# Performance work log

Hardware: AMD Instinct MI355X
Metric: run time of the kernel (lower is better)

The kernel has to match this reference:

```python
import jax, jax.numpy as jnp
import numpy as np

B, Q, K = 8, 1024, 1024
DQ, DK, DV, H = 64, 64, 64, 64
NEG = -1000000.0


def setup_inputs() -> dict:
    key = jax.random.key(0)
    ks = jax.random.split(key, 7)
    return {
        "queries": jax.random.normal(ks[0], (B, Q, DQ), dtype=jnp.float32),
        "keys": jax.random.normal(ks[1], (B, K, DK), dtype=jnp.float32),
        "values": jax.random.normal(ks[2], (B, K, DV), dtype=jnp.float32),
        "valid_lens": jax.random.randint(ks[3], (B,), 1, K + 1, dtype=jnp.int64).astype(jnp.int32),
        # learned params (LazyLinear, no bias)
        "W_q": jax.random.normal(ks[4], (DQ, H), dtype=jnp.float32) / np.sqrt(DQ),
        "W_k": jax.random.normal(ks[5], (DK, H), dtype=jnp.float32) / np.sqrt(DK),
        "w_v": jax.random.normal(ks[6], (H,), dtype=jnp.float32) / np.sqrt(H),
    }


def reference(queries, keys, values, valid_lens, W_q, W_k, w_v):
    q = jnp.einsum("bqd,dh->bqh", queries, W_q)            # [B,Q,H]
    k = jnp.einsum("bkd,dh->bkh", keys, W_k)               # [B,K,H]
    # broadcast-add + tanh materializes [B,Q,K,H] (faithful to original)
    features = jnp.tanh(q[:, :, None, :] + k[:, None, :, :])
    scores = jnp.einsum("bqkh,h->bqk", features, w_v)      # [B,Q,K]
    # masked softmax: valid_lens is 1-D -> broadcast over query rows
    mask = jnp.arange(scores.shape[-1])[None, None, :] < valid_lens[:, None, None]
    scores = jnp.where(mask, scores, NEG)
    attn = jax.nn.softmax(scores, axis=-1)                 # [B,Q,K]
    return jnp.einsum("bqk,bkv->bqv", attn, values)        # [B,Q,DV]
```

## Files before the change

kernel.cpp:

```cpp
#include <hip/hip_runtime.h>

#define BDIM 8
#define QDIM 1024
#define KDIM 1024
#define HDIM 64
#define KTPC 2
#define MAXCH 8

constexpr float kLog2e = 1.4426950408889634f;
constexpr float kC2 = 2.0f * kLog2e;

__global__ __launch_bounds__(256) void proj_both(
    const float* __restrict__ queries, const float* __restrict__ keys,
    const float* __restrict__ Wq, const float* __restrict__ Wk,
    float* __restrict__ eq, float* __restrict__ ek) {
  const int bid = blockIdx.x;
  const bool isK = bid >= 256;
  const float* X = isK ? keys : queries;
  const float* W = isK ? Wk : Wq;
  float* Y = isK ? ek : eq;
  const long long base = (long long)(bid & 255) * 32 * 64;

  __shared__ __align__(16) float xs[32][68];
  __shared__ __align__(16) float ws[64][64];
  const int t = threadIdx.x;
  {
    const int r = t >> 4, sl = t & 15;
#pragma unroll
    for (int i = 0; i < 2; ++i)
      *(float4*)&xs[r + i * 16][sl * 4] =
          *(const float4*)&X[base + (long long)(r + i * 16) * 64 + sl * 4];
#pragma unroll
    for (int i = 0; i < 4; ++i)
      *(float4*)&ws[r + i * 16][sl * 4] =
          *(const float4*)&W[(r + i * 16) * 64 + sl * 4];
  }
  __syncthreads();

  const int r = t >> 3;
  const int c0 = (t & 7) * 8;
  float acc[8];
#pragma unroll
  for (int j = 0; j < 8; ++j) acc[j] = 0.0f;

#pragma unroll 8
  for (int d = 0; d < 64; ++d) {
    const float xv = xs[r][d];
#pragma unroll
    for (int j4 = 0; j4 < 2; ++j4) {
      float4 w4 = *(float4*)&ws[d][c0 + j4 * 4];
      acc[j4 * 4 + 0] = fmaf(xv, w4.x, acc[j4 * 4 + 0]);
      acc[j4 * 4 + 1] = fmaf(xv, w4.y, acc[j4 * 4 + 1]);
      acc[j4 * 4 + 2] = fmaf(xv, w4.z, acc[j4 * 4 + 2]);
      acc[j4 * 4 + 3] = fmaf(xv, w4.w, acc[j4 * 4 + 3]);
    }
  }
#pragma unroll
  for (int j4 = 0; j4 < 2; ++j4) {
    float4 o = make_float4(
        fminf(__builtin_amdgcn_exp2f(acc[j4 * 4 + 0] * kC2), 32768.0f),
        fminf(__builtin_amdgcn_exp2f(acc[j4 * 4 + 1] * kC2), 32768.0f),
        fminf(__builtin_amdgcn_exp2f(acc[j4 * 4 + 2] * kC2), 32768.0f),
        fminf(__builtin_amdgcn_exp2f(acc[j4 * 4 + 3] * kC2), 32768.0f));
    *(float4*)&Y[base + (long long)r * 64 + c0 + j4 * 4] = o;
  }
}

__global__ __launch_bounds__(256, 4) void fused_kernel(
    const float* __restrict__ eqp, const float* __restrict__ ekp,
    const float* __restrict__ vglob, const float* __restrict__ wv,
    const int* __restrict__ vlens, float* __restrict__ part_o,
    float* __restrict__ part_l) {
  int pre[9];
  pre[0] = 0;
#pragma unroll
  for (int bb = 0; bb < 8; ++bb) {
    int nt = (vlens[bb] + 63) >> 6;
    nt = nt < 16 ? nt : 16;
    const int nch = (nt + KTPC - 1) / KTPC;
    pre[bb + 1] = pre[bb] + (nch << 6);
  }
  const int g = blockIdx.x;
  if (g >= pre[8]) return;
  int b = 0;
#pragma unroll
  for (int i = 0; i < 7; ++i) b += (g >= pre[i + 1]);
  const int local = g - pre[b];
  const int qt = local & 63;
  const int ch = local >> 6;
  const int q0 = qt * 16;
  const int vlen = vlens[b];
  int nt = (vlen + 63) >> 6;
  nt = nt < 16 ? nt : 16;
  const int kt0 = ch * KTPC;
  const int ktend = (kt0 + KTPC < nt) ? kt0 + KTPC : nt;

  __shared__ __align__(16) float qs[16][64];
  __shared__ __align__(16) float ks[64][64];
  __shared__ __align__(16) float vs[64][64];
  __shared__ __align__(16) float ps[16][64];
  const int t = threadIdx.x;
  const int tq = t >> 4;
  const int kg = t & 15;
  const int kbs = kg << 2;
  const int key0 = ((kbs + 0) ^ kg) & 15;
  const int key1 = ((kbs + 1) ^ kg) & 15;
  const int key2 = ((kbs + 2) ^ kg) & 15;
  const int key3 = ((kbs + 3) ^ kg) & 15;

  float sumw = 0.0f, sumabs = 0.0f;
#pragma unroll
  for (int h = 0; h < 64; ++h) {
    const float w = wv[h];
    sumw += w;
    sumabs += fabsf(w);
  }
  const float sbias = sumw - sumabs;

  {
    const int r = t >> 4, sl = t & 15;
    *(float4*)&qs[r][sl * 4] =
        *(const float4*)&eqp[(long long)(b * QDIM + q0 + r) * 64 + sl * 4];
  }

  float4 o4 = make_float4(0.0f, 0.0f, 0.0f, 0.0f);
  float l = 0.0f;

  for (int kt = kt0; kt < ktend; ++kt) {
    __syncthreads();
#pragma unroll
    for (int i = 0; i < 4; ++i) {
      const int f = i * 256 + t;
      const int k = f >> 4, sl = f & 15;
      const int key = (k ^ (k >> 2)) & 15;
      const long long grow = (long long)(b * KDIM + kt * 64 + k) * 64 + sl * 4;
      *(float4*)&ks[k][(sl ^ key) * 4] = *(const float4*)&ekp[grow];
      *(float4*)&vs[k][sl * 4] = *(const float4*)&vglob[grow];
    }
    __syncthreads();

    float acc0 = 0.0f, acc1 = 0.0f, acc2 = 0.0f, acc3 = 0.0f;
    float4 qA, kA0, kA1, kA2, kA3;
    float4 qB, kB0, kB1, kB2, kB3;

#define LOAD_STAGE(QF, K0, K1, K2, K3, H)                  \
  QF = *(const float4*)&qs[tq][(H) * 4];                   \
  K0 = *(const float4*)&ks[kbs + 0][((H) ^ key0) * 4];     \
  K1 = *(const float4*)&ks[kbs + 1][((H) ^ key1) * 4];     \
  K2 = *(const float4*)&ks[kbs + 2][((H) ^ key2) * 4];     \
  K3 = *(const float4*)&ks[kbs + 3][((H) ^ key3) * 4];

#define QUAD(ACC, QF, KF, W0, W1, W2, W3)                  \
  {                                                        \
    const float u0 = fmaf(QF.x, KF.x, 1.0f);               \
    const float u1 = fmaf(QF.y, KF.y, 1.0f);               \
    const float u2 = fmaf(QF.z, KF.z, 1.0f);               \
    const float u3 = fmaf(QF.w, KF.w, 1.0f);               \
    const float d01 = u0 * u1;                             \
    const float d23 = u2 * u3;                             \
    const float n01 = fmaf(W1, u0, W0 * u1);               \
    const float n23 = fmaf(W3, u2, W2 * u3);               \
    const float num = fmaf(n23, d01, n01 * d23);           \
    ACC = fmaf(num, __builtin_amdgcn_rcpf(d01 * d23), ACC);\
  }

#define COMP_STAGE(QF, K0, K1, K2, K3, H)                  \
  {                                                        \
    const float w0 = wv[(H) * 4 + 0];                      \
    const float w1 = wv[(H) * 4 + 1];                      \
    const float w2 = wv[(H) * 4 + 2];                      \
    const float w3 = wv[(H) * 4 + 3];                      \
    QUAD(acc0, QF, K0, w0, w1, w2, w3)                     \
    QUAD(acc1, QF, K1, w0, w1, w2, w3)                     \
    QUAD(acc2, QF, K2, w0, w1, w2, w3)                     \
    QUAD(acc3, QF, K3, w0, w1, w2, w3)                     \
  }

    LOAD_STAGE(qA, kA0, kA1, kA2, kA3, 0)
#pragma unroll
    for (int h = 0; h < 16; h += 2) {
      LOAD_STAGE(qB, kB0, kB1, kB2, kB3, h + 1)
      COMP_STAGE(qA, kA0, kA1, kA2, kA3, h)
      if (h + 2 < 16) LOAD_STAGE(qA, kA0, kA1, kA2, kA3, h + 2)
      COMP_STAGE(qB, kB0, kB1, kB2, kB3, h + 1)
    }
#undef LOAD_STAGE
#undef COMP_STAGE
#undef QUAD

    const int kgl = kt * 64 + kbs;
    float s0 = fmaf(-2.0f, acc0, sbias);
    float s1 = fmaf(-2.0f, acc1, sbias);
    float s2 = fmaf(-2.0f, acc2, sbias);
    float s3 = fmaf(-2.0f, acc3, sbias);
    s0 = (kgl + 0 < vlen) ? s0 : -3.0e38f;
    s1 = (kgl + 1 < vlen) ? s1 : -3.0e38f;
    s2 = (kgl + 2 < vlen) ? s2 : -3.0e38f;
    s3 = (kgl + 3 < vlen) ? s3 : -3.0e38f;
    const float p0 = __builtin_amdgcn_exp2f(s0 * kLog2e);
    const float p1 = __builtin_amdgcn_exp2f(s1 * kLog2e);
    const float p2 = __builtin_amdgcn_exp2f(s2 * kLog2e);
    const float p3 = __builtin_amdgcn_exp2f(s3 * kLog2e);
    l += (p0 + p1) + (p2 + p3);
    *(float4*)&ps[tq][(((kg + tq) & 15)) * 4] = make_float4(p0, p1, p2, p3);

#pragma unroll 4
    for (int k4 = 0; k4 < 16; ++k4) {
      const int kk = (k4 + tq) & 15;
      const float4 p4 = *(const float4*)&ps[tq][((kk + tq) & 15) * 4];
      const float pw[4] = {p4.x, p4.y, p4.z, p4.w};
#pragma unroll
      for (int e = 0; e < 4; ++e) {
        const float4 vv = *(const float4*)&vs[kk * 4 + e][kbs];
        o4.x = fmaf(pw[e], vv.x, o4.x);
        o4.y = fmaf(pw[e], vv.y, o4.y);
        o4.z = fmaf(pw[e], vv.z, o4.z);
        o4.w = fmaf(pw[e], vv.w, o4.w);
      }
    }
  }

#pragma unroll
  for (int s = 1; s < 16; s <<= 1) l += __shfl_xor(l, s, 64);
  *(float4*)&part_o[((long long)g * 16 + tq) * 64 + kbs] = o4;
  if (kg == 0) part_l[g * 16 + tq] = l;
}

__global__ __launch_bounds__(256) void combine_kernel(
    const float* __restrict__ part_o, const float* __restrict__ part_l,
    const int* __restrict__ vlens, float* __restrict__ out) {
  int pre[8], nchv[8];
  int run = 0;
#pragma unroll
  for (int bb = 0; bb < 8; ++bb) {
    int nt = (vlens[bb] + 63) >> 6;
    nt = nt < 16 ? nt : 16;
    nchv[bb] = (nt + KTPC - 1) / KTPC;
    pre[bb] = run;
    run += nchv[bb] << 6;
  }
  const int t = threadIdx.x;
  const int row = blockIdx.x * 4 + (t >> 6);
  const int lane = t & 63;
  const int b = row >> 10;
  const int q = row & (QDIM - 1);
  const int qt = q >> 4;
  const int tq = q & 15;
  const int nch = nchv[b];
  const int slot0 = pre[b] + qt;

  float L = 0.0f, acc = 0.0f;
#pragma unroll
  for (int c = 0; c < MAXCH; ++c) {
    if (c < nch) {
      L += part_l[(slot0 + (c << 6)) * 16 + tq];
      acc += part_o[((long long)(slot0 + (c << 6)) * 16 + tq) * 64 + lane];
    }
  }
  out[(long long)row * 64 + lane] = acc * __builtin_amdgcn_rcpf(L);
}

extern "C" void kernel_launch(void* const* d_in, const int* in_sizes, int n_in,
                              void* d_out, int out_size, void* d_ws, size_t ws_size,
                              hipStream_t stream) {
  const float* queries = (const float*)d_in[0];
  const float* keys    = (const float*)d_in[1];
  const float* values  = (const float*)d_in[2];
  const int*   vlens   = (const int*)d_in[3];
  const float* Wq      = (const float*)d_in[4];
  const float* Wk      = (const float*)d_in[5];
  const float* wv      = (const float*)d_in[6];
  float* out = (float*)d_out;

  float* eq     = (float*)d_ws;
  float* ek     = eq + (size_t)BDIM * QDIM * HDIM;
  float* part_o = ek + (size_t)BDIM * KDIM * HDIM;
  float* part_l = part_o + (size_t)4096 * 16 * 64;

  proj_both<<<dim3(512), 256, 0, stream>>>(queries, keys, Wq, Wk, eq, ek);
  fused_kernel<<<dim3(4096), 256, 0, stream>>>(eq, ek, values, wv, vlens,
                                               part_o, part_l);
  combine_kernel<<<dim3(BDIM * QDIM / 4), 256, 0, stream>>>(part_o, part_l,
                                                            vlens, out);
}
```

Before: 54.85 us.

## Process two query rows per thread to reuse K and V tiles

Each block of the fused kernel now handles 32 query rows instead of 16, so every thread computes two rows against the same loaded key and value fragments. This halves the number of blocks and the global loads of K/V tiles per query, and amortizes shared-memory key reads across two rows. In exchange register pressure rises, so the occupancy hint drops from 4 to 3 blocks per CU, and fewer blocks are launched. The combine kernel and workspace indexing are updated to the new 32-row layout.

Result: slower. 58.08 us (+5.9%).

```diff
diff --git a/kernel.cpp b/kernel.cpp
--- a/kernel.cpp
+++ b/kernel.cpp
@@ -66,7 +66,7 @@
   }
 }
 
-__global__ __launch_bounds__(256, 4) void fused_kernel(
+__global__ __launch_bounds__(256, 3) void fused_kernel(
     const float* __restrict__ eqp, const float* __restrict__ ekp,
     const float* __restrict__ vglob, const float* __restrict__ wv,
     const int* __restrict__ vlens, float* __restrict__ part_o,
@@ -78,7 +78,7 @@
     int nt = (vlens[bb] + 63) >> 6;
     nt = nt < 16 ? nt : 16;
     const int nch = (nt + KTPC - 1) / KTPC;
-    pre[bb + 1] = pre[bb] + (nch << 6);
+    pre[bb + 1] = pre[bb] + (nch << 5);
   }
   const int g = blockIdx.x;
   if (g >= pre[8]) return;
@@ -86,27 +86,29 @@
 #pragma unroll
   for (int i = 0; i < 7; ++i) b += (g >= pre[i + 1]);
   const int local = g - pre[b];
-  const int qt = local & 63;
-  const int ch = local >> 6;
-  const int q0 = qt * 16;
+  const int qt = local & 31;
+  const int ch = local >> 5;
+  const int q0 = qt * 32;
   const int vlen = vlens[b];
   int nt = (vlen + 63) >> 6;
   nt = nt < 16 ? nt : 16;
   const int kt0 = ch * KTPC;
   const int ktend = (kt0 + KTPC < nt) ? kt0 + KTPC : nt;
 
-  __shared__ __align__(16) float qs[16][64];
+  __shared__ __align__(16) float qs[32][68];
   __shared__ __align__(16) float ks[64][64];
   __shared__ __align__(16) float vs[64][64];
-  __shared__ __align__(16) float ps[16][64];
+  __shared__ __align__(16) float ps[32][64];
   const int t = threadIdx.x;
-  const int tq = t >> 4;
+  const int tq2 = t >> 4;
+  const int r0 = tq2, r1 = tq2 + 16;
   const int kg = t & 15;
   const int kbs = kg << 2;
   const int key0 = ((kbs + 0) ^ kg) & 15;
   const int key1 = ((kbs + 1) ^ kg) & 15;
   const int key2 = ((kbs + 2) ^ kg) & 15;
   const int key3 = ((kbs + 3) ^ kg) & 15;
+  const int pcol = (kg + r0) & 15;
 
   float sumw = 0.0f, sumabs = 0.0f;
 #pragma unroll
@@ -118,13 +120,18 @@
   const float sbias = sumw - sumabs;
 
   {
-    const int r = t >> 4, sl = t & 15;
-    *(float4*)&qs[r][sl * 4] =
-        *(const float4*)&eqp[(long long)(b * QDIM + q0 + r) * 64 + sl * 4];
-  }
-
-  float4 o4 = make_float4(0.0f, 0.0f, 0.0f, 0.0f);
-  float l = 0.0f;
+#pragma unroll
+    for (int i = 0; i < 2; ++i) {
+      const int f = i * 256 + t;
+      const int r = f >> 4, sl = f & 15;
+      *(float4*)&qs[r][sl * 4] =
+          *(const float4*)&eqp[(long long)(b * QDIM + q0 + r) * 64 + sl * 4];
+    }
+  }
+
+  float4 oA = make_float4(0.0f, 0.0f, 0.0f, 0.0f);
+  float4 oB = make_float4(0.0f, 0.0f, 0.0f, 0.0f);
+  float lA = 0.0f, lB = 0.0f;
 
   for (int kt = kt0; kt < ktend; ++kt) {
     __syncthreads();
@@ -139,12 +146,14 @@
     }
     __syncthreads();
 
-    float acc0 = 0.0f, acc1 = 0.0f, acc2 = 0.0f, acc3 = 0.0f;
-    float4 qA, kA0, kA1, kA2, kA3;
-    float4 qB, kB0, kB1, kB2, kB3;
-
-#define LOAD_STAGE(QF, K0, K1, K2, K3, H)                  \
-  QF = *(const float4*)&qs[tq][(H) * 4];                   \
+    float accA0 = 0.0f, accA1 = 0.0f, accA2 = 0.0f, accA3 = 0.0f;
+    float accB0 = 0.0f, accB1 = 0.0f, accB2 = 0.0f, accB3 = 0.0f;
+    float4 qA0, qB0, kA0, kA1, kA2, kA3;
+    float4 qA1, qB1, kB0, kB1, kB2, kB3;
+
+#define LOAD_STAGE(QA, QB, K0, K1, K2, K3, H)              \
+  QA = *(const float4*)&qs[r0][(H) * 4];                   \
+  QB = *(const float4*)&qs[r1][(H) * 4];                   \
   K0 = *(const float4*)&ks[kbs + 0][((H) ^ key0) * 4];     \
   K1 = *(const float4*)&ks[kbs + 1][((H) ^ key1) * 4];     \
   K2 = *(const float4*)&ks[kbs + 2][((H) ^ key2) * 4];     \
@@ -164,66 +173,90 @@
     ACC = fmaf(num, __builtin_amdgcn_rcpf(d01 * d23), ACC);\
   }
 
-#define COMP_STAGE(QF, K0, K1, K2, K3, H)                  \
+#define COMP_STAGE(QA, QB, K0, K1, K2, K3, H)              \
   {                                                        \
     const float w0 = wv[(H) * 4 + 0];                      \
     const float w1 = wv[(H) * 4 + 1];                      \
     const float w2 = wv[(H) * 4 + 2];                      \
     const float w3 = wv[(H) * 4 + 3];                      \
-    QUAD(acc0, QF, K0, w0, w1, w2, w3)                     \
-    QUAD(acc1, QF, K1, w0, w1, w2, w3)                     \
-    QUAD(acc2, QF, K2, w0, w1, w2, w3)                     \
-    QUAD(acc3, QF, K3, w0, w1, w2, w3)                     \
-  }
-
-    LOAD_STAGE(qA, kA0, kA1, kA2, kA3, 0)
+    QUAD(accA0, QA, K0, w0, w1, w2, w3)                    \
+    QUAD(accA1, QA, K1, w0, w1, w2, w3)                    \
+    QUAD(accA2, QA, K2, w0, w1, w2, w3)                    \
+    QUAD(accA3, QA, K3, w0, w1, w2, w3)                    \
+    QUAD(accB0, QB, K0, w0, w1, w2, w3)                    \
+    QUAD(accB1, QB, K1, w0, w1, w2, w3)                    \
+    QUAD(accB2, QB, K2, w0, w1, w2, w3)                    \
+    QUAD(accB3, QB, K3, w0, w1, w2, w3)                    \
+  }
+
+    LOAD_STAGE(qA0, qA1, kA0, kA1, kA2, kA3, 0)
 #pragma unroll
     for (int h = 0; h < 16; h += 2) {
-      LOAD_STAGE(qB, kB0, kB1, kB2, kB3, h + 1)
-      COMP_STAGE(qA, kA0, kA1, kA2, kA3, h)
-      if (h + 2 < 16) LOAD_STAGE(qA, kA0, kA1, kA2, kA3, h + 2)
-      COMP_STAGE(qB, kB0, kB1, kB2, kB3, h + 1)
+      LOAD_STAGE(qB0, qB1, kB0, kB1, kB2, kB3, h + 1)
+      COMP_STAGE(qA0, qA1, kA0, kA1, kA2, kA3, h)
+      if (h + 2 < 16) LOAD_STAGE(qA0, qA1, kA0, kA1, kA2, kA3, h + 2)
+      COMP_STAGE(qB0, qB1, kB0, kB1, kB2, kB3, h + 1)
     }
 #undef LOAD_STAGE
 #undef COMP_STAGE
 #undef QUAD
 
     const int kgl = kt * 64 + kbs;
-    float s0 = fmaf(-2.0f, acc0, sbias);
-    float s1 = fmaf(-2.0f, acc1, sbias);
-    float s2 = fmaf(-2.0f, acc2, sbias);
-    float s3 = fmaf(-2.0f, acc3, sbias);
-    s0 = (kgl + 0 < vlen) ? s0 : -3.0e38f;
-    s1 = (kgl + 1 < vlen) ? s1 : -3.0e38f;
-    s2 = (kgl + 2 < vlen) ? s2 : -3.0e38f;
-    s3 = (kgl + 3 < vlen) ? s3 : -3.0e38f;
-    const float p0 = __builtin_amdgcn_exp2f(s0 * kLog2e);
-    const float p1 = __builtin_amdgcn_exp2f(s1 * kLog2e);
-    const float p2 = __builtin_amdgcn_exp2f(s2 * kLog2e);
-    const float p3 = __builtin_amdgcn_exp2f(s3 * kLog2e);
-    l += (p0 + p1) + (p2 + p3);
-    *(float4*)&ps[tq][(((kg + tq) & 15)) * 4] = make_float4(p0, p1, p2, p3);
+    const bool v0 = kgl + 0 < vlen, v1 = kgl + 1 < vlen;
+    const bool v2 = kgl + 2 < vlen, v3 = kgl + 3 < vlen;
+    float sA0 = v0 ? fmaf(-2.0f, accA0, sbias) : -3.0e38f;
+    float sA1 = v1 ? fmaf(-2.0f, accA1, sbias) : -3.0e38f;
+    float sA2 = v2 ? fmaf(-2.0f, accA2, sbias) : -3.0e38f;
+    float sA3 = v3 ? fmaf(-2.0f, accA3, sbias) : -3.0e38f;
+    float sB0 = v0 ? fmaf(-2.0f, accB0, sbias) : -3.0e38f;
+    float sB1 = v1 ? fmaf(-2.0f, accB1, sbias) : -3.0e38f;
+    float sB2 = v2 ? fmaf(-2.0f, accB2, sbias) : -3.0e38f;
+    float sB3 = v3 ? fmaf(-2.0f, accB3, sbias) : -3.0e38f;
+    const float pA0 = __builtin_amdgcn_exp2f(sA0 * kLog2e);
+    const float pA1 = __builtin_amdgcn_exp2f(sA1 * kLog2e);
+    const float pA2 = __builtin_amdgcn_exp2f(sA2 * kLog2e);
+    const float pA3 = __builtin_amdgcn_exp2f(sA3 * kLog2e);
+    const float pB0 = __builtin_amdgcn_exp2f(sB0 * kLog2e);
+    const float pB1 = __builtin_amdgcn_exp2f(sB1 * kLog2e);
+    const float pB2 = __builtin_amdgcn_exp2f(sB2 * kLog2e);
+    const float pB3 = __builtin_amdgcn_exp2f(sB3 * kLog2e);
+    lA += (pA0 + pA1) + (pA2 + pA3);
+    lB += (pB0 + pB1) + (pB2 + pB3);
+    *(float4*)&ps[r0][pcol * 4] = make_float4(pA0, pA1, pA2, pA3);
+    *(float4*)&ps[r1][pcol * 4] = make_float4(pB0, pB1, pB2, pB3);
 
 #pragma unroll 4
     for (int k4 = 0; k4 < 16; ++k4) {
-      const int kk = (k4 + tq) & 15;
-      const float4 p4 = *(const float4*)&ps[tq][((kk + tq) & 15) * 4];
-      const float pw[4] = {p4.x, p4.y, p4.z, p4.w};
+      const float4 pa = *(const float4*)&ps[r0][((k4 + r0) & 15) * 4];
+      const float4 pb = *(const float4*)&ps[r1][((k4 + r1) & 15) * 4];
+      const float pwA[4] = {pa.x, pa.y, pa.z, pa.w};
+      const float pwB[4] = {pb.x, pb.y, pb.z, pb.w};
 #pragma unroll
       for (int e = 0; e < 4; ++e) {
-        const float4 vv = *(const float4*)&vs[kk * 4 + e][kbs];
-        o4.x = fmaf(pw[e], vv.x, o4.x);
-        o4.y = fmaf(pw[e], vv.y, o4.y);
-        o4.z = fmaf(pw[e], vv.z, o4.z);
-        o4.w = fmaf(pw[e], vv.w, o4.w);
+        const float4 vv = *(const float4*)&vs[k4 * 4 + e][kbs];
+        oA.x = fmaf(pwA[e], vv.x, oA.x);
+        oA.y = fmaf(pwA[e], vv.y, oA.y);
+        oA.z = fmaf(pwA[e], vv.z, oA.z);
+        oA.w = fmaf(pwA[e], vv.w, oA.w);
+        oB.x = fmaf(pwB[e], vv.x, oB.x);
+        oB.y = fmaf(pwB[e], vv.y, oB.y);
+        oB.z = fmaf(pwB[e], vv.z, oB.z);
+        oB.w = fmaf(pwB[e], vv.w, oB.w);
       }
     }
   }
 
 #pragma unroll
-  for (int s = 1; s < 16; s <<= 1) l += __shfl_xor(l, s, 64);
-  *(float4*)&part_o[((long long)g * 16 + tq) * 64 + kbs] = o4;
-  if (kg == 0) part_l[g * 16 + tq] = l;
+  for (int s = 1; s < 16; s <<= 1) {
+    lA += __shfl_xor(lA, s, 64);
+    lB += __shfl_xor(lB, s, 64);
+  }
+  *(float4*)&part_o[((long long)g * 32 + r0) * 64 + kbs] = oA;
+  *(float4*)&part_o[((long long)g * 32 + r1) * 64 + kbs] = oB;
+  if (kg == 0) {
+    part_l[g * 32 + r0] = lA;
+    part_l[g * 32 + r1] = lB;
+  }
 }
 
 __global__ __launch_bounds__(256) void combine_kernel(
@@ -237,15 +270,15 @@
     nt = nt < 16 ? nt : 16;
     nchv[bb] = (nt + KTPC - 1) / KTPC;
     pre[bb] = run;
-    run += nchv[bb] << 6;
+    run += nchv[bb] << 5;
   }
   const int t = threadIdx.x;
   const int row = blockIdx.x * 4 + (t >> 6);
   const int lane = t & 63;
   const int b = row >> 10;
   const int q = row & (QDIM - 1);
-  const int qt = q >> 4;
-  const int tq = q & 15;
+  const int qt = q >> 5;
+  const int tq = q & 31;
   const int nch = nchv[b];
   const int slot0 = pre[b] + qt;
 
@@ -253,8 +286,8 @@
 #pragma unroll
   for (int c = 0; c < MAXCH; ++c) {
     if (c < nch) {
-      L += part_l[(slot0 + (c << 6)) * 16 + tq];
-      acc += part_o[((long long)(slot0 + (c << 6)) * 16 + tq) * 64 + lane];
+      L += part_l[(slot0 + (c << 5)) * 32 + tq];
+      acc += part_o[((long long)(slot0 + (c << 5)) * 32 + tq) * 64 + lane];
     }
   }
   out[(long long)row * 64 + lane] = acc * __builtin_amdgcn_rcpf(L);
@@ -275,10 +308,10 @@
   float* eq     = (float*)d_ws;
   float* ek     = eq + (size_t)BDIM * QDIM * HDIM;
   float* part_o = ek + (size_t)BDIM * KDIM * HDIM;
-  float* part_l = part_o + (size_t)4096 * 16 * 64;
+  float* part_l = part_o + (size_t)2048 * 32 * 64;
 
   proj_both<<<dim3(512), 256, 0, stream>>>(queries, keys, Wq, Wk, eq, ek);
-  fused_kernel<<<dim3(4096), 256, 0, stream>>>(eq, ek, values, wv, vlens,
+  fused_kernel<<<dim3(2048), 256, 0, stream>>>(eq, ek, values, wv, vlens,
                                                part_o, part_l);
   combine_kernel<<<dim3(BDIM * QDIM / 4), 256, 0, stream>>>(part_o, part_l,
                                                             vlens, out);
```

## Read K and V tiles straight from global memory instead of LDS staging

Applied to the files above, without the earlier changes.

The shared-memory tiles for projected keys and values are removed. Each thread now loads its K rows and V columns directly from global memory into register double-buffers, and the two per-tile __syncthreads barriers go away. The probability scratch row is shared only among the 16 threads of one wavefront, so no block barrier is needed for it. This trades LDS traffic and barrier stalls for redundant, strided global/L1 loads: all 16 query rows in a block reload the same K/V data, which may stress cache bandwidth and latency.

After: 182.1 us. 3.32x slower.

```diff
diff --git a/kernel.cpp b/kernel.cpp
--- a/kernel.cpp
+++ b/kernel.cpp
@@ -95,18 +95,13 @@
   const int kt0 = ch * KTPC;
   const int ktend = (kt0 + KTPC < nt) ? kt0 + KTPC : nt;
 
-  __shared__ __align__(16) float qs[16][64];
-  __shared__ __align__(16) float ks[64][64];
-  __shared__ __align__(16) float vs[64][64];
+  __shared__ __align__(16) float qs[16][68];
   __shared__ __align__(16) float ps[16][64];
   const int t = threadIdx.x;
   const int tq = t >> 4;
   const int kg = t & 15;
   const int kbs = kg << 2;
-  const int key0 = ((kbs + 0) ^ kg) & 15;
-  const int key1 = ((kbs + 1) ^ kg) & 15;
-  const int key2 = ((kbs + 2) ^ kg) & 15;
-  const int key3 = ((kbs + 3) ^ kg) & 15;
+  const int pcol = (kg + tq) & 15;
 
   float sumw = 0.0f, sumabs = 0.0f;
 #pragma unroll
@@ -122,33 +117,24 @@
     *(float4*)&qs[r][sl * 4] =
         *(const float4*)&eqp[(long long)(b * QDIM + q0 + r) * 64 + sl * 4];
   }
+  __syncthreads();
 
   float4 o4 = make_float4(0.0f, 0.0f, 0.0f, 0.0f);
   float l = 0.0f;
 
   for (int kt = kt0; kt < ktend; ++kt) {
-    __syncthreads();
-#pragma unroll
-    for (int i = 0; i < 4; ++i) {
-      const int f = i * 256 + t;
-      const int k = f >> 4, sl = f & 15;
-      const int key = (k ^ (k >> 2)) & 15;
-      const long long grow = (long long)(b * KDIM + kt * 64 + k) * 64 + sl * 4;
-      *(float4*)&ks[k][(sl ^ key) * 4] = *(const float4*)&ekp[grow];
-      *(float4*)&vs[k][sl * 4] = *(const float4*)&vglob[grow];
-    }
-    __syncthreads();
+    const float* pK = ekp + ((long long)(b * KDIM + kt * 64 + kbs)) * 64;
+    const float* pV = vglob + ((long long)(b * KDIM + kt * 64)) * 64 + kbs;
 
     float acc0 = 0.0f, acc1 = 0.0f, acc2 = 0.0f, acc3 = 0.0f;
-    float4 qA, kA0, kA1, kA2, kA3;
-    float4 qB, kB0, kB1, kB2, kB3;
-
-#define LOAD_STAGE(QF, K0, K1, K2, K3, H)                  \
-  QF = *(const float4*)&qs[tq][(H) * 4];                   \
-  K0 = *(const float4*)&ks[kbs + 0][((H) ^ key0) * 4];     \
-  K1 = *(const float4*)&ks[kbs + 1][((H) ^ key1) * 4];     \
-  K2 = *(const float4*)&ks[kbs + 2][((H) ^ key2) * 4];     \
-  K3 = *(const float4*)&ks[kbs + 3][((H) ^ key3) * 4];
+    float4 kA0, kA1, kA2, kA3;
+    float4 kB0, kB1, kB2, kB3;
+
+#define LOADG_K(K0, K1, K2, K3, H)               \
+  K0 = *(const float4*)(pK + 0 * 64 + (H) * 4);  \
+  K1 = *(const float4*)(pK + 1 * 64 + (H) * 4);  \
+  K2 = *(const float4*)(pK + 2 * 64 + (H) * 4);  \
+  K3 = *(const float4*)(pK + 3 * 64 + (H) * 4);
 
 #define QUAD(ACC, QF, KF, W0, W1, W2, W3)                  \
   {                                                        \
@@ -164,60 +150,85 @@
     ACC = fmaf(num, __builtin_amdgcn_rcpf(d01 * d23), ACC);\
   }
 
-#define COMP_STAGE(QF, K0, K1, K2, K3, H)                  \
+#define COMP_STAGE(K0, K1, K2, K3, H)                      \
   {                                                        \
+    const float4 q4 = *(const float4*)&qs[tq][(H) * 4];    \
     const float w0 = wv[(H) * 4 + 0];                      \
     const float w1 = wv[(H) * 4 + 1];                      \
     const float w2 = wv[(H) * 4 + 2];                      \
     const float w3 = wv[(H) * 4 + 3];                      \
-    QUAD(acc0, QF, K0, w0, w1, w2, w3)                     \
-    QUAD(acc1, QF, K1, w0, w1, w2, w3)                     \
-    QUAD(acc2, QF, K2, w0, w1, w2, w3)                     \
-    QUAD(acc3, QF, K3, w0, w1, w2, w3)                     \
-  }
-
-    LOAD_STAGE(qA, kA0, kA1, kA2, kA3, 0)
+    QUAD(acc0, q4, K0, w0, w1, w2, w3)                     \
+    QUAD(acc1, q4, K1, w0, w1, w2, w3)                     \
+    QUAD(acc2, q4, K2, w0, w1, w2, w3)                     \
+    QUAD(acc3, q4, K3, w0, w1, w2, w3)                     \
+  }
+
+    LOADG_K(kA0, kA1, kA2, kA3, 0)
+    LOADG_K(kB0, kB1, kB2, kB3, 1)
 #pragma unroll
     for (int h = 0; h < 16; h += 2) {
-      LOAD_STAGE(qB, kB0, kB1, kB2, kB3, h + 1)
-      COMP_STAGE(qA, kA0, kA1, kA2, kA3, h)
-      if (h + 2 < 16) LOAD_STAGE(qA, kA0, kA1, kA2, kA3, h + 2)
-      COMP_STAGE(qB, kB0, kB1, kB2, kB3, h + 1)
-    }
-#undef LOAD_STAGE
+      COMP_STAGE(kA0, kA1, kA2, kA3, h)
+      if (h + 2 < 16) LOADG_K(kA0, kA1, kA2, kA3, h + 2)
+      COMP_STAGE(kB0, kB1, kB2, kB3, h + 1)
+      if (h + 3 < 16) LOADG_K(kB0, kB1, kB2, kB3, h + 3)
+    }
+#undef LOADG_K
 #undef COMP_STAGE
 #undef QUAD
 
     const int kgl = kt * 64 + kbs;
-    float s0 = fmaf(-2.0f, acc0, sbias);
-    float s1 = fmaf(-2.0f, acc1, sbias);
-    float s2 = fmaf(-2.0f, acc2, sbias);
-    float s3 = fmaf(-2.0f, acc3, sbias);
-    s0 = (kgl + 0 < vlen) ? s0 : -3.0e38f;
-    s1 = (kgl + 1 < vlen) ? s1 : -3.0e38f;
-    s2 = (kgl + 2 < vlen) ? s2 : -3.0e38f;
-    s3 = (kgl + 3 < vlen) ? s3 : -3.0e38f;
+    float s0 = (kgl + 0 < vlen) ? fmaf(-2.0f, acc0, sbias) : -3.0e38f;
+    float s1 = (kgl + 1 < vlen) ? fmaf(-2.0f, acc1, sbias) : -3.0e38f;
+    float s2 = (kgl + 2 < vlen) ? fmaf(-2.0f, acc2, sbias) : -3.0e38f;
+    float s3 = (kgl + 3 < vlen) ? fmaf(-2.0f, acc3, sbias) : -3.0e38f;
     const float p0 = __builtin_amdgcn_exp2f(s0 * kLog2e);
     const float p1 = __builtin_amdgcn_exp2f(s1 * kLog2e);
     const float p2 = __builtin_amdgcn_exp2f(s2 * kLog2e);
     const float p3 = __builtin_amdgcn_exp2f(s3 * kLog2e);
     l += (p0 + p1) + (p2 + p3);
-    *(float4*)&ps[tq][(((kg + tq) & 15)) * 4] = make_float4(p0, p1, p2, p3);
-
-#pragma unroll 4
-    for (int k4 = 0; k4 < 16; ++k4) {
-      const int kk = (k4 + tq) & 15;
-      const float4 p4 = *(const float4*)&ps[tq][((kk + tq) & 15) * 4];
-      const float pw[4] = {p4.x, p4.y, p4.z, p4.w};
-#pragma unroll
-      for (int e = 0; e < 4; ++e) {
-        const float4 vv = *(const float4*)&vs[kk * 4 + e][kbs];
-        o4.x = fmaf(pw[e], vv.x, o4.x);
-        o4.y = fmaf(pw[e], vv.y, o4.y);
-        o4.z = fmaf(pw[e], vv.z, o4.z);
-        o4.w = fmaf(pw[e], vv.w, o4.w);
-      }
-    }
+    *(float4*)&ps[tq][pcol * 4] = make_float4(p0, p1, p2, p3);
+
+    float4 vA0, vA1, vA2, vA3;
+    float4 vB0, vB1, vB2, vB3;
+
+#define LOADG_V(V0, V1, V2, V3, K4)                    \
+  V0 = *(const float4*)(pV + ((K4) * 4 + 0) * 64);     \
+  V1 = *(const float4*)(pV + ((K4) * 4 + 1) * 64);     \
+  V2 = *(const float4*)(pV + ((K4) * 4 + 2) * 64);     \
+  V3 = *(const float4*)(pV + ((K4) * 4 + 3) * 64);
+
+#define PV_STAGE(V0, V1, V2, V3, K4)                           \
+  {                                                            \
+    const float4 p4 = *(const float4*)&ps[tq][(((K4) + tq) & 15) * 4]; \
+    o4.x = fmaf(p4.x, V0.x, o4.x);                             \
+    o4.y = fmaf(p4.x, V0.y, o4.y);                             \
+    o4.z = fmaf(p4.x, V0.z, o4.z);                             \
+    o4.w = fmaf(p4.x, V0.w, o4.w);                             \
+    o4.x = fmaf(p4.y, V1.x, o4.x);                             \
+    o4.y = fmaf(p4.y, V1.y, o4.y);                             \
+    o4.z = fmaf(p4.y, V1.z, o4.z);                             \
+    o4.w = fmaf(p4.y, V1.w, o4.w);                             \
+    o4.x = fmaf(p4.z, V2.x, o4.x);                             \
+    o4.y = fmaf(p4.z, V2.y, o4.y);                             \
+    o4.z = fmaf(p4.z, V2.z, o4.z);                             \
+    o4.w = fmaf(p4.z, V2.w, o4.w);                             \
+    o4.x = fmaf(p4.w, V3.x, o4.x);                             \
+    o4.y = fmaf(p4.w, V3.y, o4.y);                             \
+    o4.z = fmaf(p4.w, V3.z, o4.z);                             \
+    o4.w = fmaf(p4.w, V3.w, o4.w);                             \
+  }
+
+    LOADG_V(vA0, vA1, vA2, vA3, 0)
+    LOADG_V(vB0, vB1, vB2, vB3, 1)
+#pragma unroll
+    for (int k4 = 0; k4 < 16; k4 += 2) {
+      PV_STAGE(vA0, vA1, vA2, vA3, k4 + 0)
+      if (k4 + 2 < 16) LOADG_V(vA0, vA1, vA2, vA3, k4 + 2)
+      PV_STAGE(vB0, vB1, vB2, vB3, k4 + 1)
+      if (k4 + 3 < 16) LOADG_V(vB0, vB1, vB2, vB3, k4 + 3)
+    }
+#undef LOADG_V
+#undef PV_STAGE
   }
 
 #pragma unroll
```
